# Optimization experiments

Hardware: AMD Instinct MI355X
Metric: run time of the kernel (lower is better)

The kernel has to match this reference:

```python
import jax, jax.numpy as jnp
import numpy as np

D_MODEL = 1024
N_HEADS = 16
HEAD = D_MODEL // N_HEADS  # 64


def setup_inputs() -> dict:
    key = jax.random.key(0)
    ks = jax.random.split(key, 9)
    s = 1.0 / np.sqrt(D_MODEL)
    x = jax.random.normal(ks[0], (2, 2048, D_MODEL), dtype=jnp.float32)
    Wq = jax.random.uniform(ks[1], (N_HEADS, D_MODEL, HEAD), jnp.float32, -s, s)
    bq = jax.random.uniform(ks[2], (N_HEADS, HEAD), jnp.float32, -s, s)
    Wk = jax.random.uniform(ks[3], (N_HEADS, D_MODEL, HEAD), jnp.float32, -s, s)
    bk = jax.random.uniform(ks[4], (N_HEADS, HEAD), jnp.float32, -s, s)
    Wv = jax.random.uniform(ks[5], (N_HEADS, D_MODEL, HEAD), jnp.float32, -s, s)
    bv = jax.random.uniform(ks[6], (N_HEADS, HEAD), jnp.float32, -s, s)
    Wo = jax.random.uniform(ks[7], (D_MODEL, D_MODEL), jnp.float32, -s, s)
    bo = jax.random.uniform(ks[8], (D_MODEL,), jnp.float32, -s, s)
    return {"x": x, "Wq": Wq, "bq": bq, "Wk": Wk, "bk": bk,
            "Wv": Wv, "bv": bv, "Wo": Wo, "bo": bo}


def reference(x, Wq, bq, Wk, bk, Wv, bv, Wo, bo):
    # Per-head projections, vectorized over heads: [B,S,D] x [H,D,h] -> [B,H,S,h]
    Q = jnp.einsum('bsd,hdk->bhsk', x, Wq) + bq[None, :, None, :]
    K = jnp.einsum('bsd,hdk->bhsk', x, Wk) + bk[None, :, None, :]
    V = jnp.einsum('bsd,hdk->bhsk', x, Wv) + bv[None, :, None, :]
    scores = jnp.einsum('bhqk,bhsk->bhqs', Q, K) / jnp.sqrt(jnp.float32(HEAD))
    attn = jax.nn.softmax(scores, axis=-1)  # dropout is identity in eval mode
    out = jnp.einsum('bhqs,bhsk->bhqk', attn, V)  # [B,H,S,h]
    B, H, S, h = out.shape
    out = out.transpose(0, 2, 1, 3).reshape(B, S, H * h)  # concat heads -> [B,S,D]
    return out @ Wo.T + bo if False else jnp.einsum('bsd,ed->bse', out, Wo.T.T) + bo
```

## Files before the change

kernel.cpp:

```cpp
#include <hip/hip_runtime.h>
#include <hip/hip_bf16.h>

typedef unsigned short u16;
typedef short short8 __attribute__((ext_vector_type(8)));
typedef float floatx4 __attribute__((ext_vector_type(4)));

#define MFMA16(a, b, c) __builtin_amdgcn_mfma_f32_16x16x32_bf16((a), (b), (c), 0, 0, 0)

union U128u { uint4 q; u16 s[8]; };

__device__ __forceinline__ u16 f2bf(float f) {
  union { float f; unsigned u; } v; v.f = f;
  unsigned r = v.u + 0x7fffu + ((v.u >> 16) & 1u);
  return (u16)(r >> 16);
}

__device__ __forceinline__ unsigned pk2(float hi, float lo) {
  union { float f; unsigned u; } a, b;
  a.f = hi; b.f = lo;
  return __builtin_amdgcn_perm(a.u + 0x8000u, b.u + 0x8000u, 0x07060302u);
}

__device__ __forceinline__ float fexp2(float x) {
#if __has_builtin(__builtin_amdgcn_exp2f)
  return __builtin_amdgcn_exp2f(x);
#else
  return exp2f(x);
#endif
}

__device__ __forceinline__ void async16(const u16* g, u16* l) {
  __builtin_amdgcn_global_load_lds(
      (const __attribute__((address_space(1))) unsigned int*)g,
      (__attribute__((address_space(3))) unsigned int*)l, 16, 0, 0);
}


__global__ __launch_bounds__(256) void prep_all(
    const float* __restrict__ x, const float* __restrict__ Wo,
    const float* __restrict__ Wq, const float* __restrict__ bq,
    const float* __restrict__ Wk, const float* __restrict__ bk,
    const float* __restrict__ Wv, const float* __restrict__ bv,
    u16* __restrict__ Xb, u16* __restrict__ Wob,
    u16* __restrict__ Wt, float* __restrict__ ball) {
  int bid = blockIdx.x;
  int tid = threadIdx.x;
  if (bid < 5120) {
    const float* src = bid < 4096 ? x : Wo;
    u16* dst = bid < 4096 ? Xb : Wob;
    int i = (bid < 4096 ? bid : bid - 4096) * 256 + tid;
    float4 v = ((const float4*)src)[i];
    union { unsigned long long ll; u16 s[4]; } o;
    o.s[0] = f2bf(v.x); o.s[1] = f2bf(v.y); o.s[2] = f2bf(v.z); o.s[3] = f2bf(v.w);
    ((unsigned long long*)dst)[i] = o.ll;
    return;
  }
  int id = (bid - 5120) * 256 + tid;
  int kk4 = id & 15;
  int d = (id >> 4) & 1023;
  int h = (id >> 14) & 15;
  int wsel = id >> 18;
  const float* W = wsel == 0 ? Wq : (wsel == 1 ? Wk : Wv);
  float4 v = *(const float4*)(W + ((size_t)(h * 1024 + d)) * 64 + kk4 * 4);
  int nb = wsel * 1024 + h * 64 + kk4 * 4;
  Wt[(size_t)(nb + 0) * 1024 + d] = f2bf(v.x);
  Wt[(size_t)(nb + 1) * 1024 + d] = f2bf(v.y);
  Wt[(size_t)(nb + 2) * 1024 + d] = f2bf(v.z);
  Wt[(size_t)(nb + 3) * 1024 + d] = f2bf(v.w);
  if (id < 3072) {
    int ws2 = id >> 10, hk = id & 1023;
    const float* bsrc = ws2 == 0 ? bq : (ws2 == 1 ? bk : bv);
    ball[id] = bsrc[hk];
  }
}

__global__ __launch_bounds__(256) void transpose_v(const u16* __restrict__ QKV,
                                                   u16* __restrict__ Vtc) {
  __shared__ u16 t[64][65];
  int tid = threadIdx.x;
  int bh = blockIdx.y, b = bh >> 4, h = bh & 15;
  int s0 = blockIdx.x * 64;
  int v0 = blockIdx.x * 4;
  {
    int r = tid >> 2, c0 = (tid & 3) * 16;
    const u16* src = QKV + (size_t)(b * 2048 + s0 + r) * 3072 + 2048 + h * 64 + c0;
    U128u a, c;
    a.q = *(const uint4*)src;
    c.q = *(const uint4*)(src + 8);
#pragma unroll
    for (int j = 0; j < 8; ++j) { t[r][c0 + j] = a.s[j]; t[r][c0 + 8 + j] = c.s[j]; }
  }
  __syncthreads();
  {
    int g = tid;
#pragma unroll
    for (int gg = 0; gg < 2; ++gg, g += 256) {
      int d = g & 63, o = (g >> 6) & 1, vloc = g >> 7;
      int sl = vloc * 16 + o * 8;
      U128u out;
#pragma unroll
      for (int k = 0; k < 8; ++k) out.s[k] = t[sl + k][d];
      u16* dst = Vtc + (((size_t)(bh * 128 + v0 + vloc) * 2 + o) * 64 + d) * 8;
      *(uint4*)dst = out.q;
    }
  }
}


__device__ __forceinline__ void store_out(u16* p, float v) { *p = f2bf(v); }
__device__ __forceinline__ void store_out(float* p, float v) { *p = v; }

template <int BN, typename OutT>
__global__ __launch_bounds__(256) void gemm_bt(
    const u16* __restrict__ A, const u16* __restrict__ B,
    const float* __restrict__ bias, OutT* __restrict__ C,
    int M, int N, int K, int scaleNend, float scaleVal) {
  constexpr int TN = BN / 32;
  __shared__ __attribute__((aligned(16))) u16 As[128 * 32];
  __shared__ __attribute__((aligned(16))) u16 Bs[BN * 32];
  const int tid = threadIdx.x;
  const int w = tid >> 6, lane = tid & 63;
  const int l15 = lane & 15, l4 = lane >> 4;
  const int lin = blockIdx.x;
  const int xcd = lin & 7, sblk = lin >> 3;
  const int bm = xcd * 4 + (sblk & 3);
  const int bn = sblk >> 2;
  const int wm = (w & 1) * 64, wn = (w >> 1) * (BN / 2);

  floatx4 acc[4][TN];
#pragma unroll
  for (int i = 0; i < 4; ++i)
#pragma unroll
    for (int j = 0; j < TN; ++j) acc[i][j] = (floatx4){0.f, 0.f, 0.f, 0.f};

  for (int k0 = 0; k0 < K; k0 += 32) {
    __syncthreads();
#pragma unroll
    for (int j = 0; j < 2; ++j) {
      int i = j * 256 + tid;
      int row = i >> 2, ko = (i & 3) * 8;
      async16(A + (size_t)(bm * 128 + row) * K + k0 + ko, As + (j * 256 + w * 64) * 8);
    }
#pragma unroll
    for (int j = 0; j < BN / 64; ++j) {
      int i = j * 256 + tid;
      int row = i >> 2, ko = (i & 3) * 8;
      async16(B + (size_t)(bn * BN + row) * K + k0 + ko, Bs + (j * 256 + w * 64) * 8);
    }
    __syncthreads();
    short8 af[4], bf[TN];
#pragma unroll
    for (int t = 0; t < 4; ++t)
      af[t] = *(const short8*)(As + (wm + t * 16 + l15) * 32 + l4 * 8);
#pragma unroll
    for (int t = 0; t < TN; ++t)
      bf[t] = *(const short8*)(Bs + (wn + t * 16 + l15) * 32 + l4 * 8);
#pragma unroll
    for (int tm = 0; tm < 4; ++tm)
#pragma unroll
      for (int tn = 0; tn < TN; ++tn) acc[tm][tn] = MFMA16(af[tm], bf[tn], acc[tm][tn]);
  }

#pragma unroll
  for (int tn = 0; tn < TN; ++tn) {
    int col = bn * BN + wn + tn * 16 + l15;
    float bv = bias[col];
    float sc = (col < scaleNend) ? scaleVal : 1.0f;
#pragma unroll
    for (int tm = 0; tm < 4; ++tm) {
      int row0 = bm * 128 + wm + tm * 16 + l4 * 4;
#pragma unroll
      for (int r = 0; r < 4; ++r) {
        float v = (acc[tm][tn][r] + bv) * sc;
        store_out(C + (size_t)(row0 + r) * N + col, v);
      }
    }
  }
}


__global__ __launch_bounds__(256, 2) void attn_kernel(const u16* __restrict__ QKV,
                                                      const u16* __restrict__ Vtc,
                                                      u16* __restrict__ O) {
  __shared__ __attribute__((aligned(16))) u16 Ks[8192];
  __shared__ __attribute__((aligned(16))) u16 Vs[8192];
  __shared__ __attribute__((aligned(16))) u16 Ps[4 * 2432];
  const int tid = threadIdx.x;
  const int w = tid >> 6, lane = tid & 63;
  const int l15 = lane & 15, l4 = lane >> 4;
  const int lin = blockIdx.x;
  const int xcd = lin & 7, sblk = lin >> 3;
  const int bh = xcd * 4 + (sblk & 3);
  const int q0 = (sblk >> 2) * 128;
  const int b = bh >> 4, h = bh & 15;

  u16* const Pw = Ps + w * 2432;

  short8 qf[2][2];
  {
    const u16* Qb = QKV + (size_t)(b * 2048 + q0 + w * 32) * 3072 + h * 64;
#pragma unroll
    for (int tq = 0; tq < 2; ++tq)
#pragma unroll
      for (int s = 0; s < 2; ++s)
        qf[tq][s] = *(const short8*)(Qb + (size_t)(tq * 16 + l15) * 3072 + s * 32 + l4 * 8);
  }

  floatx4 Oacc[2][4];
#pragma unroll
  for (int i = 0; i < 2; ++i)
#pragma unroll
    for (int j = 0; j < 4; ++j) Oacc[i][j] = (floatx4){0.f, 0.f, 0.f, 0.f};
  float lpart[2] = {0.f, 0.f};

  const u16* const Kb = QKV + (size_t)(b * 2048) * 3072 + 1024 + h * 64;
  const u16* const Vb = Vtc + (size_t)bh * 131072;

  const int kseg = lane >> 3;
  const int koct = (lane & 7) ^ (kseg & 7);

  for (int kt = 0; kt < 16; ++kt) {
    __syncthreads();
#pragma unroll
    for (int r = 0; r < 4; ++r) {
      int seg = r * 4 + w;
      async16(Kb + (size_t)(kt * 128 + seg * 8 + kseg) * 3072 + koct * 8, Ks + seg * 512);
      async16(Vb + (size_t)kt * 8192 + seg * 512 + lane * 8, Vs + seg * 512);
    }
    __syncthreads();

#pragma unroll
    for (int hh = 0; hh < 2; ++hh) {
#pragma unroll
      for (int tk = 0; tk < 4; ++tk) {
        int krow = hh * 64 + tk * 16 + l15;
        int swk = l15 & 7;
        short8 kf0 = *(const short8*)(Ks + krow * 64 + (l4 ^ swk) * 8);
        short8 kf1 = *(const short8*)(Ks + krow * 64 + ((4 + l4) ^ swk) * 8);
#pragma unroll
        for (int tq = 0; tq < 2; ++tq) {
          floatx4 s = (floatx4){0.f, 0.f, 0.f, 0.f};
          s = MFMA16(kf0, qf[tq][0], s);
          s = MFMA16(kf1, qf[tq][1], s);
          float p0 = fexp2(s[0]), p1 = fexp2(s[1]), p2 = fexp2(s[2]), p3 = fexp2(s[3]);
          lpart[tq] += (p0 + p1) + (p2 + p3);
          unsigned lo = pk2(p1, p0), hi = pk2(p3, p2);
          *(unsigned long long*)(Pw + (size_t)(tq * 16 + l15) * 76 + tk * 16 + l4 * 4) =
              ((unsigned long long)hi << 32) | lo;
        }
      }
      short8 pf[2][2];
#pragma unroll
      for (int tq = 0; tq < 2; ++tq)
#pragma unroll
        for (int kc = 0; kc < 2; ++kc)
          pf[tq][kc] = *(const short8*)(Pw + (size_t)(tq * 16 + l15) * 76 + kc * 32 + l4 * 8);
#pragma unroll
      for (int td = 0; td < 4; ++td)
#pragma unroll
        for (int kc = 0; kc < 2; ++kc) {
          short8 vf = *(const short8*)(Vs + (hh * 8 + kc * 4 + l4) * 512 + (td * 16 + l15) * 8);
#pragma unroll
          for (int tq = 0; tq < 2; ++tq) Oacc[tq][td] = MFMA16(pf[tq][kc], vf, Oacc[tq][td]);
        }
    }
  }

  float linv[2];
#pragma unroll
  for (int tq = 0; tq < 2; ++tq) {
    float l = lpart[tq];
    l += __shfl_xor(l, 16);
    l += __shfl_xor(l, 32);
    linv[tq] = 1.0f / l;
  }
  float iv[2][4];
#pragma unroll
  for (int tq = 0; tq < 2; ++tq)
#pragma unroll
    for (int r = 0; r < 4; ++r) iv[tq][r] = __shfl(linv[tq], l4 * 4 + r);

  u16* Ob = O + (size_t)(b * 2048 + q0 + w * 32) * 1024 + h * 64;
#pragma unroll
  for (int tq = 0; tq < 2; ++tq)
#pragma unroll
    for (int td = 0; td < 4; ++td)
#pragma unroll
      for (int r = 0; r < 4; ++r)
        Ob[(size_t)(tq * 16 + l4 * 4 + r) * 1024 + td * 16 + l15] =
            f2bf(Oacc[tq][td][r] * iv[tq][r]);
}


extern "C" void kernel_launch(void* const* d_in, const int* in_sizes, int n_in,
                              void* d_out, int out_size, void* d_ws, size_t ws_size,
                              hipStream_t stream) {
  const float* x  = (const float*)d_in[0];
  const float* Wq = (const float*)d_in[1];
  const float* bq = (const float*)d_in[2];
  const float* Wk = (const float*)d_in[3];
  const float* bk = (const float*)d_in[4];
  const float* Wv = (const float*)d_in[5];
  const float* bv = (const float*)d_in[6];
  const float* Wo = (const float*)d_in[7];
  const float* bo = (const float*)d_in[8];

  char* p = (char*)d_ws;
  u16* Xb   = (u16*)p; p += (size_t)4096 * 1024 * 2;
  u16* Wt   = (u16*)p; p += (size_t)3072 * 1024 * 2;
  u16* QKV  = (u16*)p; p += (size_t)4096 * 3072 * 2;
  u16* Vtc  = (u16*)p; p += (size_t)32 * 128 * 2 * 64 * 8 * 2;
  u16* Ob   = (u16*)p; p += (size_t)4096 * 1024 * 2;
  u16* Wob  = (u16*)p; p += (size_t)1024 * 1024 * 2;
  float* ball = (float*)p; p += 3072 * sizeof(float);

  const float qscale = 0.125f * 1.4426950408889634f;

  prep_all<<<8192, 256, 0, stream>>>(x, Wo, Wq, bq, Wk, bk, Wv, bv, Xb, Wob, Wt, ball);
  gemm_bt<128, u16><<<768, 256, 0, stream>>>(Xb, Wt, ball, QKV,
                                             4096, 3072, 1024, 1024, qscale);
  transpose_v<<<dim3(32, 32), 256, 0, stream>>>(QKV, Vtc);
  attn_kernel<<<512, 256, 0, stream>>>(QKV, Vtc, Ob);
  gemm_bt<64, float><<<512, 256, 0, stream>>>(Ob, Wob, bo, (float*)d_out,
                                              4096, 1024, 1024, 0, 1.0f);
}
```

Measured before the change: 227.2 us.

## Split attention over two key halves and add combine kernel

After: 226.2 us. About the same (-0.4%).

```diff
diff --git a/kernel.cpp b/kernel.cpp
--- a/kernel.cpp
+++ b/kernel.cpp
@@ -13,6 +13,11 @@
   union { float f; unsigned u; } v; v.f = f;
   unsigned r = v.u + 0x7fffu + ((v.u >> 16) & 1u);
   return (u16)(r >> 16);
+}
+
+__device__ __forceinline__ float bf2f(u16 s) {
+  union { unsigned u; float f; } v; v.u = ((unsigned)s) << 16;
+  return v.f;
 }
 
 __device__ __forceinline__ unsigned pk2(float hi, float lo) {
@@ -179,11 +184,12 @@
 }
 
 
-__global__ __launch_bounds__(256, 2) void attn_kernel(const u16* __restrict__ QKV,
+__global__ __launch_bounds__(256, 4) void attn_kernel(const u16* __restrict__ QKV,
                                                       const u16* __restrict__ Vtc,
-                                                      u16* __restrict__ O) {
-  __shared__ __attribute__((aligned(16))) u16 Ks[8192];
-  __shared__ __attribute__((aligned(16))) u16 Vs[8192];
+                                                      u16* __restrict__ Op,
+                                                      float* __restrict__ Lp) {
+  __shared__ __attribute__((aligned(16))) u16 Ks[4096];
+  __shared__ __attribute__((aligned(16))) u16 Vs[4096];
   __shared__ __attribute__((aligned(16))) u16 Ps[4 * 2432];
   const int tid = threadIdx.x;
   const int w = tid >> 6, lane = tid & 63;
@@ -191,7 +197,9 @@
   const int lin = blockIdx.x;
   const int xcd = lin & 7, sblk = lin >> 3;
   const int bh = xcd * 4 + (sblk & 3);
-  const int q0 = (sblk >> 2) * 128;
+  const int rem = sblk >> 2;
+  const int q0 = (rem & 15) * 128;
+  const int ks = rem >> 4;
   const int b = bh >> 4, h = bh & 15;
 
   u16* const Pw = Ps + w * 2432;
@@ -213,82 +221,96 @@
     for (int j = 0; j < 4; ++j) Oacc[i][j] = (floatx4){0.f, 0.f, 0.f, 0.f};
   float lpart[2] = {0.f, 0.f};
 
-  const u16* const Kb = QKV + (size_t)(b * 2048) * 3072 + 1024 + h * 64;
-  const u16* const Vb = Vtc + (size_t)bh * 131072;
+  const u16* const Kb = QKV + (size_t)(b * 2048 + ks * 1024) * 3072 + 1024 + h * 64;
+  const u16* const Vb = Vtc + (size_t)bh * 131072 + (size_t)ks * 65536;
 
   const int kseg = lane >> 3;
-  const int koct = (lane & 7) ^ (kseg & 7);
+  const int koct = (lane & 7) ^ kseg;
 
   for (int kt = 0; kt < 16; ++kt) {
     __syncthreads();
 #pragma unroll
-    for (int r = 0; r < 4; ++r) {
+    for (int r = 0; r < 2; ++r) {
       int seg = r * 4 + w;
-      async16(Kb + (size_t)(kt * 128 + seg * 8 + kseg) * 3072 + koct * 8, Ks + seg * 512);
-      async16(Vb + (size_t)kt * 8192 + seg * 512 + lane * 8, Vs + seg * 512);
+      async16(Kb + (size_t)(kt * 64 + seg * 8 + kseg) * 3072 + koct * 8, Ks + seg * 512);
+      async16(Vb + (size_t)kt * 4096 + seg * 512 + lane * 8, Vs + seg * 512);
     }
     __syncthreads();
 
 #pragma unroll
-    for (int hh = 0; hh < 2; ++hh) {
-#pragma unroll
-      for (int tk = 0; tk < 4; ++tk) {
-        int krow = hh * 64 + tk * 16 + l15;
-        int swk = l15 & 7;
-        short8 kf0 = *(const short8*)(Ks + krow * 64 + (l4 ^ swk) * 8);
-        short8 kf1 = *(const short8*)(Ks + krow * 64 + ((4 + l4) ^ swk) * 8);
-#pragma unroll
-        for (int tq = 0; tq < 2; ++tq) {
-          floatx4 s = (floatx4){0.f, 0.f, 0.f, 0.f};
-          s = MFMA16(kf0, qf[tq][0], s);
-          s = MFMA16(kf1, qf[tq][1], s);
-          float p0 = fexp2(s[0]), p1 = fexp2(s[1]), p2 = fexp2(s[2]), p3 = fexp2(s[3]);
-          lpart[tq] += (p0 + p1) + (p2 + p3);
-          unsigned lo = pk2(p1, p0), hi = pk2(p3, p2);
-          *(unsigned long long*)(Pw + (size_t)(tq * 16 + l15) * 76 + tk * 16 + l4 * 4) =
-              ((unsigned long long)hi << 32) | lo;
-        }
+    for (int tk = 0; tk < 4; ++tk) {
+      int krow = tk * 16 + l15;
+      int swk = l15 & 7;
+      short8 kf0 = *(const short8*)(Ks + krow * 64 + (l4 ^ swk) * 8);
+      short8 kf1 = *(const short8*)(Ks + krow * 64 + ((4 + l4) ^ swk) * 8);
+#pragma unroll
+      for (int tq = 0; tq < 2; ++tq) {
+        floatx4 s = (floatx4){0.f, 0.f, 0.f, 0.f};
+        s = MFMA16(kf0, qf[tq][0], s);
+        s = MFMA16(kf1, qf[tq][1], s);
+        float p0 = fexp2(s[0]), p1 = fexp2(s[1]), p2 = fexp2(s[2]), p3 = fexp2(s[3]);
+        lpart[tq] += (p0 + p1) + (p2 + p3);
+        unsigned lo = pk2(p1, p0), hi = pk2(p3, p2);
+        *(unsigned long long*)(Pw + (size_t)(tq * 16 + l15) * 76 + tk * 16 + l4 * 4) =
+            ((unsigned long long)hi << 32) | lo;
       }
-      short8 pf[2][2];
-#pragma unroll
-      for (int tq = 0; tq < 2; ++tq)
-#pragma unroll
-        for (int kc = 0; kc < 2; ++kc)
-          pf[tq][kc] = *(const short8*)(Pw + (size_t)(tq * 16 + l15) * 76 + kc * 32 + l4 * 8);
-#pragma unroll
-      for (int td = 0; td < 4; ++td)
-#pragma unroll
-        for (int kc = 0; kc < 2; ++kc) {
-          short8 vf = *(const short8*)(Vs + (hh * 8 + kc * 4 + l4) * 512 + (td * 16 + l15) * 8);
-#pragma unroll
-          for (int tq = 0; tq < 2; ++tq) Oacc[tq][td] = MFMA16(pf[tq][kc], vf, Oacc[tq][td]);
-        }
-    }
-  }
-
-  float linv[2];
+    }
+    short8 pf[2][2];
+#pragma unroll
+    for (int tq = 0; tq < 2; ++tq)
+#pragma unroll
+      for (int kc = 0; kc < 2; ++kc)
+        pf[tq][kc] = *(const short8*)(Pw + (size_t)(tq * 16 + l15) * 76 + kc * 32 + l4 * 8);
+#pragma unroll
+    for (int td = 0; td < 4; ++td)
+#pragma unroll
+      for (int kc = 0; kc < 2; ++kc) {
+        short8 vf = *(const short8*)(Vs + (kc * 4 + l4) * 512 + (td * 16 + l15) * 8);
+#pragma unroll
+        for (int tq = 0; tq < 2; ++tq) Oacc[tq][td] = MFMA16(pf[tq][kc], vf, Oacc[tq][td]);
+      }
+  }
+
+  float lr[2];
 #pragma unroll
   for (int tq = 0; tq < 2; ++tq) {
     float l = lpart[tq];
     l += __shfl_xor(l, 16);
     l += __shfl_xor(l, 32);
-    linv[tq] = 1.0f / l;
-  }
-  float iv[2][4];
+    lr[tq] = l;
+  }
+  if (l4 == 0) {
+#pragma unroll
+    for (int tq = 0; tq < 2; ++tq)
+      Lp[(size_t)(ks * 32 + bh) * 2048 + q0 + w * 32 + tq * 16 + l15] = lr[tq];
+  }
+
+  u16* Opb = Op + (size_t)ks * 4194304 + (size_t)(b * 2048 + q0 + w * 32) * 1024 + h * 64;
 #pragma unroll
   for (int tq = 0; tq < 2; ++tq)
 #pragma unroll
-    for (int r = 0; r < 4; ++r) iv[tq][r] = __shfl(linv[tq], l4 * 4 + r);
-
-  u16* Ob = O + (size_t)(b * 2048 + q0 + w * 32) * 1024 + h * 64;
-#pragma unroll
-  for (int tq = 0; tq < 2; ++tq)
-#pragma unroll
     for (int td = 0; td < 4; ++td)
 #pragma unroll
       for (int r = 0; r < 4; ++r)
-        Ob[(size_t)(tq * 16 + l4 * 4 + r) * 1024 + td * 16 + l15] =
-            f2bf(Oacc[tq][td][r] * iv[tq][r]);
+        Opb[(size_t)(tq * 16 + l4 * 4 + r) * 1024 + td * 16 + l15] = f2bf(Oacc[tq][td][r]);
+}
+
+
+__global__ __launch_bounds__(256) void combine_kernel(const u16* __restrict__ Op,
+                                                      const float* __restrict__ Lp,
+                                                      u16* __restrict__ Ob) {
+  int i = blockIdx.x * 256 + threadIdx.x;
+  int t = i >> 8, c4 = i & 255, h = c4 >> 4;
+  ushort4 a = ((const ushort4*)Op)[i];
+  ushort4 c = ((const ushort4*)Op)[1048576 + i];
+  int li = ((t >> 11) * 16 + h) * 2048 + (t & 2047);
+  float inv = 1.0f / (Lp[li] + Lp[65536 + li]);
+  float o0 = (bf2f(a.x) + bf2f(c.x)) * inv;
+  float o1 = (bf2f(a.y) + bf2f(c.y)) * inv;
+  float o2 = (bf2f(a.z) + bf2f(c.z)) * inv;
+  float o3 = (bf2f(a.w) + bf2f(c.w)) * inv;
+  unsigned lo = pk2(o1, o0), hi = pk2(o3, o2);
+  ((unsigned long long*)Ob)[i] = ((unsigned long long)hi << 32) | lo;
 }
 
 
@@ -312,6 +334,8 @@
   u16* Vtc  = (u16*)p; p += (size_t)32 * 128 * 2 * 64 * 8 * 2;
   u16* Ob   = (u16*)p; p += (size_t)4096 * 1024 * 2;
   u16* Wob  = (u16*)p; p += (size_t)1024 * 1024 * 2;
+  u16* Op   = (u16*)p; p += (size_t)2 * 4096 * 1024 * 2;
+  float* Lp = (float*)p; p += (size_t)2 * 32 * 2048 * sizeof(float);
   float* ball = (float*)p; p += 3072 * sizeof(float);
 
   const float qscale = 0.125f * 1.4426950408889634f;
@@ -320,7 +344,8 @@
   gemm_bt<128, u16><<<768, 256, 0, stream>>>(Xb, Wt, ball, QKV,
                                              4096, 3072, 1024, 1024, qscale);
   transpose_v<<<dim3(32, 32), 256, 0, stream>>>(QKV, Vtc);
-  attn_kernel<<<512, 256, 0, stream>>>(QKV, Vtc, Ob);
+  attn_kernel<<<1024, 256, 0, stream>>>(QKV, Vtc, Op, Lp);
+  combine_kernel<<<4096, 256, 0, stream>>>(Op, Lp, Ob);
   gemm_bt<64, float><<<512, 256, 0, stream>>>(Ob, Wob, bo, (float*)d_out,
                                               4096, 1024, 1024, 0, 1.0f);
 }
```

## Split keys across waves in attention, reduce partial outputs through LDS

Applied to the files above, without the earlier changes.

After: 215.4 us. -5.2%, faster.

```diff
diff --git a/kernel.cpp b/kernel.cpp
--- a/kernel.cpp
+++ b/kernel.cpp
@@ -13,6 +13,11 @@
   union { float f; unsigned u; } v; v.f = f;
   unsigned r = v.u + 0x7fffu + ((v.u >> 16) & 1u);
   return (u16)(r >> 16);
+}
+
+__device__ __forceinline__ float bf2f(u16 s) {
+  union { unsigned u; float f; } v; v.u = ((unsigned)s) << 16;
+  return v.f;
 }
 
 __device__ __forceinline__ unsigned pk2(float hi, float lo) {
@@ -179,116 +184,126 @@
 }
 
 
-__global__ __launch_bounds__(256, 2) void attn_kernel(const u16* __restrict__ QKV,
+__global__ __launch_bounds__(256, 3) void attn_kernel(const u16* __restrict__ QKV,
                                                       const u16* __restrict__ Vtc,
-                                                      u16* __restrict__ O) {
-  __shared__ __attribute__((aligned(16))) u16 Ks[8192];
-  __shared__ __attribute__((aligned(16))) u16 Vs[8192];
-  __shared__ __attribute__((aligned(16))) u16 Ps[4 * 2432];
+                                                      u16* __restrict__ Ob) {
+  __shared__ __attribute__((aligned(16))) u16 lds[4 * 4736];
   const int tid = threadIdx.x;
   const int w = tid >> 6, lane = tid & 63;
   const int l15 = lane & 15, l4 = lane >> 4;
   const int lin = blockIdx.x;
   const int xcd = lin & 7, sblk = lin >> 3;
   const int bh = xcd * 4 + (sblk & 3);
-  const int q0 = (sblk >> 2) * 128;
+  const int q0 = (sblk >> 2) * 64;
   const int b = bh >> 4, h = bh & 15;
 
-  u16* const Pw = Ps + w * 2432;
-
-  short8 qf[2][2];
+  u16* const Pw = lds + w * 4736;
+
+  short8 qf[4][2];
   {
-    const u16* Qb = QKV + (size_t)(b * 2048 + q0 + w * 32) * 3072 + h * 64;
-#pragma unroll
-    for (int tq = 0; tq < 2; ++tq)
+    const u16* Qb = QKV + (size_t)(b * 2048 + q0) * 3072 + h * 64;
+#pragma unroll
+    for (int tq = 0; tq < 4; ++tq)
 #pragma unroll
       for (int s = 0; s < 2; ++s)
         qf[tq][s] = *(const short8*)(Qb + (size_t)(tq * 16 + l15) * 3072 + s * 32 + l4 * 8);
   }
 
-  floatx4 Oacc[2][4];
-#pragma unroll
-  for (int i = 0; i < 2; ++i)
+  floatx4 Oacc[4][4];
+#pragma unroll
+  for (int i = 0; i < 4; ++i)
 #pragma unroll
     for (int j = 0; j < 4; ++j) Oacc[i][j] = (floatx4){0.f, 0.f, 0.f, 0.f};
-  float lpart[2] = {0.f, 0.f};
+  float lpart[4] = {0.f, 0.f, 0.f, 0.f};
 
   const u16* const Kb = QKV + (size_t)(b * 2048) * 3072 + 1024 + h * 64;
-  const u16* const Vb = Vtc + (size_t)bh * 131072;
-
-  const int kseg = lane >> 3;
-  const int koct = (lane & 7) ^ (kseg & 7);
-
-  for (int kt = 0; kt < 16; ++kt) {
-    __syncthreads();
-#pragma unroll
-    for (int r = 0; r < 4; ++r) {
-      int seg = r * 4 + w;
-      async16(Kb + (size_t)(kt * 128 + seg * 8 + kseg) * 3072 + koct * 8, Ks + seg * 512);
-      async16(Vb + (size_t)kt * 8192 + seg * 512 + lane * 8, Vs + seg * 512);
-    }
-    __syncthreads();
-
-#pragma unroll
-    for (int hh = 0; hh < 2; ++hh) {
-#pragma unroll
-      for (int tk = 0; tk < 4; ++tk) {
-        int krow = hh * 64 + tk * 16 + l15;
-        int swk = l15 & 7;
-        short8 kf0 = *(const short8*)(Ks + krow * 64 + (l4 ^ swk) * 8);
-        short8 kf1 = *(const short8*)(Ks + krow * 64 + ((4 + l4) ^ swk) * 8);
-#pragma unroll
-        for (int tq = 0; tq < 2; ++tq) {
-          floatx4 s = (floatx4){0.f, 0.f, 0.f, 0.f};
-          s = MFMA16(kf0, qf[tq][0], s);
-          s = MFMA16(kf1, qf[tq][1], s);
-          float p0 = fexp2(s[0]), p1 = fexp2(s[1]), p2 = fexp2(s[2]), p3 = fexp2(s[3]);
-          lpart[tq] += (p0 + p1) + (p2 + p3);
-          unsigned lo = pk2(p1, p0), hi = pk2(p3, p2);
-          *(unsigned long long*)(Pw + (size_t)(tq * 16 + l15) * 76 + tk * 16 + l4 * 4) =
-              ((unsigned long long)hi << 32) | lo;
-        }
+  const u16* const Vw = Vtc + (size_t)bh * 131072 + (size_t)w * 32768;
+  const int kw0 = w * 512;
+
+  for (int c = 0; c < 16; ++c) {
+    const int key0 = kw0 + c * 32;
+    short8 kf[2][2];
+#pragma unroll
+    for (int t = 0; t < 2; ++t)
+#pragma unroll
+      for (int s = 0; s < 2; ++s)
+        kf[t][s] = *(const short8*)(Kb + (size_t)(key0 + t * 16 + l15) * 3072 + s * 32 + l4 * 8);
+    short8 vf[4];
+#pragma unroll
+    for (int td = 0; td < 4; ++td)
+      vf[td] = *(const short8*)(Vw + (size_t)c * 2048 + l4 * 512 + (td * 16 + l15) * 8);
+
+#pragma unroll
+    for (int t = 0; t < 2; ++t)
+#pragma unroll
+      for (int tq = 0; tq < 4; ++tq) {
+        floatx4 s = (floatx4){0.f, 0.f, 0.f, 0.f};
+        s = MFMA16(kf[t][0], qf[tq][0], s);
+        s = MFMA16(kf[t][1], qf[tq][1], s);
+        float p0 = fexp2(s[0]), p1 = fexp2(s[1]), p2 = fexp2(s[2]), p3 = fexp2(s[3]);
+        lpart[tq] += (p0 + p1) + (p2 + p3);
+        unsigned lo = pk2(p1, p0), hi = pk2(p3, p2);
+        *(unsigned long long*)(Pw + (size_t)(tq * 16 + l15) * 40 + t * 16 + l4 * 4) =
+            ((unsigned long long)hi << 32) | lo;
       }
-      short8 pf[2][2];
-#pragma unroll
-      for (int tq = 0; tq < 2; ++tq)
-#pragma unroll
-        for (int kc = 0; kc < 2; ++kc)
-          pf[tq][kc] = *(const short8*)(Pw + (size_t)(tq * 16 + l15) * 76 + kc * 32 + l4 * 8);
-#pragma unroll
-      for (int td = 0; td < 4; ++td)
-#pragma unroll
-        for (int kc = 0; kc < 2; ++kc) {
-          short8 vf = *(const short8*)(Vs + (hh * 8 + kc * 4 + l4) * 512 + (td * 16 + l15) * 8);
-#pragma unroll
-          for (int tq = 0; tq < 2; ++tq) Oacc[tq][td] = MFMA16(pf[tq][kc], vf, Oacc[tq][td]);
-        }
-    }
-  }
-
-  float linv[2];
-#pragma unroll
-  for (int tq = 0; tq < 2; ++tq) {
+
+    short8 pf[4];
+#pragma unroll
+    for (int tq = 0; tq < 4; ++tq)
+      pf[tq] = *(const short8*)(Pw + (size_t)(tq * 16 + l15) * 40 + l4 * 8);
+#pragma unroll
+    for (int td = 0; td < 4; ++td)
+#pragma unroll
+      for (int tq = 0; tq < 4; ++tq) Oacc[tq][td] = MFMA16(pf[tq], vf[td], Oacc[tq][td]);
+  }
+
+  float lr[4];
+#pragma unroll
+  for (int tq = 0; tq < 4; ++tq) {
     float l = lpart[tq];
     l += __shfl_xor(l, 16);
     l += __shfl_xor(l, 32);
-    linv[tq] = 1.0f / l;
-  }
-  float iv[2][4];
-#pragma unroll
-  for (int tq = 0; tq < 2; ++tq)
-#pragma unroll
-    for (int r = 0; r < 4; ++r) iv[tq][r] = __shfl(linv[tq], l4 * 4 + r);
-
-  u16* Ob = O + (size_t)(b * 2048 + q0 + w * 32) * 1024 + h * 64;
-#pragma unroll
-  for (int tq = 0; tq < 2; ++tq)
+    lr[tq] = l;
+  }
+
+#pragma unroll
+  for (int tq = 0; tq < 4; ++tq)
 #pragma unroll
     for (int td = 0; td < 4; ++td)
 #pragma unroll
       for (int r = 0; r < 4; ++r)
-        Ob[(size_t)(tq * 16 + l4 * 4 + r) * 1024 + td * 16 + l15] =
-            f2bf(Oacc[tq][td][r] * iv[tq][r]);
+        Pw[(size_t)(tq * 16 + l4 * 4 + r) * 72 + td * 16 + l15] = f2bf(Oacc[tq][td][r]);
+  if (l4 == 0) {
+    float* Lw = (float*)(Pw + 4608);
+#pragma unroll
+    for (int tq = 0; tq < 4; ++tq) Lw[tq * 16 + l15] = lr[tq];
+  }
+  __syncthreads();
+
+  {
+    int row = tid >> 2, c0 = (tid & 3) * 16;
+    float acc[16];
+#pragma unroll
+    for (int j = 0; j < 16; ++j) acc[j] = 0.f;
+    float lsum = 0.f;
+#pragma unroll
+    for (int wv = 0; wv < 4; ++wv) {
+      const u16* R = lds + wv * 4736;
+      lsum += ((const float*)(R + 4608))[row];
+      U128u x1, x2;
+      x1.q = *(const uint4*)(R + (size_t)row * 72 + c0);
+      x2.q = *(const uint4*)(R + (size_t)row * 72 + c0 + 8);
+#pragma unroll
+      for (int j = 0; j < 8; ++j) { acc[j] += bf2f(x1.s[j]); acc[8 + j] += bf2f(x2.s[j]); }
+    }
+    float inv = 1.0f / lsum;
+    U128u o1, o2;
+#pragma unroll
+    for (int j = 0; j < 8; ++j) { o1.s[j] = f2bf(acc[j] * inv); o2.s[j] = f2bf(acc[8 + j] * inv); }
+    u16* Op = Ob + (size_t)(b * 2048 + q0 + row) * 1024 + h * 64 + c0;
+    *(uint4*)Op = o1.q;
+    *(uint4*)(Op + 8) = o2.q;
+  }
 }
 
 
@@ -320,7 +335,7 @@
   gemm_bt<128, u16><<<768, 256, 0, stream>>>(Xb, Wt, ball, QKV,
                                              4096, 3072, 1024, 1024, qscale);
   transpose_v<<<dim3(32, 32), 256, 0, stream>>>(QKV, Vtc);
-  attn_kernel<<<512, 256, 0, stream>>>(QKV, Vtc, Ob);
+  attn_kernel<<<1024, 256, 0, stream>>>(QKV, Vtc, Ob);
   gemm_bt<64, float><<<512, 256, 0, stream>>>(Ob, Wob, bo, (float*)d_out,
                                               4096, 1024, 1024, 0, 1.0f);
 }
```
